# Optimization experiments

Measured on AMD Instinct MI355X. Metric: run time of the kernel, lower is better.

The kernel has to match this reference:

```python
import jax, jax.numpy as jnp
import numpy as np

N_FP = 235336   # n_fingerprint
N_WORD = 7844   # n_word
D = 10          # embed / hidden dim (hard-coded in module)
K = 23          # conv kernel 2*11+1
PAD = 11
N_ATOMS = 4096
L_WORDS = 65536


def setup_inputs() -> dict:
    key = jax.random.key(0)
    ks = jax.random.split(key, 16)
    s = 0.1  # weight init scale
    return {
        "fingerprints": jax.random.randint(ks[0], (N_ATOMS,), 0, N_FP),
        # scale adjacency so x + A@hs stays O(1) over 3 layers
        "adjacency": jax.random.uniform(ks[1], (N_ATOMS, N_ATOMS), dtype=jnp.float32) * (1.0 / N_ATOMS),
        "words": jax.random.randint(ks[2], (L_WORDS,), 0, N_WORD),
        "embed_fp": jax.random.normal(ks[3], (N_FP, D), dtype=jnp.float32) * s,
        "embed_word": jax.random.normal(ks[4], (N_WORD, D), dtype=jnp.float32) * s,
        "W_gnn_w": jax.random.normal(ks[5], (3, D, D), dtype=jnp.float32) * s,
        "W_gnn_b": jax.random.normal(ks[6], (3, D), dtype=jnp.float32) * s,
        "W_cnn_w": jax.random.normal(ks[7], (3, 1, 1, K, K), dtype=jnp.float32) * (s / K),
        "W_cnn_b": jax.random.normal(ks[8], (3,), dtype=jnp.float32) * s,
        "W_att_w": jax.random.normal(ks[9], (D, D), dtype=jnp.float32) * s,
        "W_att_b": jax.random.normal(ks[10], (D,), dtype=jnp.float32) * s,
        "W_out_w": jax.random.normal(ks[11], (3, 2 * D, 2 * D), dtype=jnp.float32) * s,
        "W_out_b": jax.random.normal(ks[12], (3, 2 * D), dtype=jnp.float32) * s,
        "W_int_w": jax.random.normal(ks[13], (2, 2 * D), dtype=jnp.float32) * s,
        "W_int_b": jax.random.normal(ks[14], (2,), dtype=jnp.float32) * s,
    }


def reference(fingerprints, adjacency, words, embed_fp, embed_word,
              W_gnn_w, W_gnn_b, W_cnn_w, W_cnn_b, W_att_w, W_att_b,
              W_out_w, W_out_b, W_int_w, W_int_b):
    # ---- Compound vector with GNN ----
    xs = embed_fp[fingerprints]                       # [N, D]
    for i in range(3):                                # fixed 3 layers
        hs = jax.nn.relu(xs @ W_gnn_w[i].T + W_gnn_b[i])
        xs = xs + adjacency @ hs                      # dense message passing
    compound = jnp.mean(xs, axis=0, keepdims=True)    # [1, D]

    # ---- Protein vector with attention-CNN ----
    ws = embed_word[words]                            # [L, D]
    t = ws[None, None]                                # [1,1,L,D] NCHW
    for i in range(3):
        t = jax.nn.relu(
            jax.lax.conv_general_dilated(t, W_cnn_w[i], (1, 1),
                                          [(PAD, PAD), (PAD, PAD)])
            + W_cnn_b[i])
    xs_p = t[0, 0]                                    # [L, D]

    h = jax.nn.relu(compound @ W_att_w.T + W_att_b)   # [1, D]
    hs_p = jax.nn.relu(xs_p @ W_att_w.T + W_att_b)    # [L, D]
    weights = jnp.tanh(h @ hs_p.T)                    # [1, L]
    ys = weights.T * hs_p                             # [L, D]
    protein = jnp.mean(ys, axis=0, keepdims=True)     # [1, D]

    # ---- Fusion MLP ----
    cat = jnp.concatenate([compound, protein], axis=1)  # [1, 2D]
    for j in range(3):
        cat = jax.nn.relu(cat @ W_out_w[j].T + W_out_b[j])
    return cat @ W_int_w.T + W_int_b                  # [1, 2]
```

## Files before the change

### kernel.cpp

```cpp
#include <hip/hip_runtime.h>
#include <math.h>

#define N_ATOMS 4096
#define L_WORDS 65536
#define DD 10
#define HALO 11

#define CONV_BLOCKS 256
#define CONV_BLOCK 256
#define GNN_BLOCKS 512
#define RPW 8
#define RPB 32
#define QCOLS 1024

__global__ __launch_bounds__(128) void gnn_embed(
    const int* __restrict__ fp, const float* __restrict__ embed_fp,
    const float* __restrict__ Wg, const float* __restrict__ bg,
    float* __restrict__ xs, float* __restrict__ hs)
{
    const int n = blockIdx.x * 128 + threadIdx.x;
    float x[DD];
    const float* e = embed_fp + (size_t)fp[n] * DD;
    #pragma unroll
    for (int d = 0; d < DD; ++d) x[d] = e[d];
    #pragma unroll
    for (int d = 0; d < DD; ++d) xs[d * N_ATOMS + n] = x[d];
    #pragma unroll
    for (int d = 0; d < DD; ++d) {
        float v = bg[d];
        #pragma unroll
        for (int k = 0; k < DD; ++k) v += Wg[d * DD + k] * x[k];
        hs[d * N_ATOMS + n] = fmaxf(v, 0.f);
    }
}

__global__ __launch_bounds__(128) void gnn_prep(
    const float* __restrict__ xs_in, const float* __restrict__ part,
    const float* __restrict__ Wg, const float* __restrict__ bg,
    float* __restrict__ xs_out, float* __restrict__ hs)
{
    const int n = blockIdx.x * 128 + threadIdx.x;
    float x[DD];
    #pragma unroll
    for (int d = 0; d < DD; ++d) {
        float v = xs_in[d * N_ATOMS + n];
        #pragma unroll
        for (int q = 0; q < 4; ++q)
            v += part[((size_t)q * DD + d) * N_ATOMS + n];
        x[d] = v;
        xs_out[d * N_ATOMS + n] = v;
    }
    #pragma unroll
    for (int d = 0; d < DD; ++d) {
        float v = bg[d];
        #pragma unroll
        for (int k = 0; k < DD; ++k) v += Wg[d * DD + k] * x[k];
        hs[d * N_ATOMS + n] = fmaxf(v, 0.f);
    }
}

__global__ __launch_bounds__(256, 3) void fused_layer(
    const float* __restrict__ A,
    const float* __restrict__ hs,
    float* __restrict__ part,
    const float* __restrict__ tin, const int* __restrict__ words,
    const float* __restrict__ embed_word, const float* __restrict__ w,
    const float* __restrict__ bptr, float* __restrict__ tout)
{
    __shared__ float sh[DD * QCOLS];
    const int tid = threadIdx.x;

    if (blockIdx.x < CONV_BLOCKS) {
        float* s = sh;
        const int l0 = blockIdx.x * CONV_BLOCK;
        for (int idx = tid; idx < (CONV_BLOCK + 2 * HALO) * DD; idx += CONV_BLOCK) {
            int rr = idx / DD, d = idx - rr * DD;
            int gr = l0 - HALO + rr;
            float v = 0.f;
            if (gr >= 0 && gr < L_WORDS) {
                if (tin) v = tin[(size_t)gr * DD + d];
                else     v = embed_word[(size_t)words[gr] * DD + d];
            }
            s[rr * 11 + d] = v;
        }
        __syncthreads();

        const float bias = *bptr;
        float acc[DD];
        #pragma unroll
        for (int d = 0; d < DD; ++d) acc[d] = bias;
        for (int i = 0; i < 23; ++i) {
            float row[DD];
            const float* sr = &s[(tid + i) * 11];
            #pragma unroll
            for (int c = 0; c < DD; ++c) row[c] = sr[c];
            #pragma unroll
            for (int d = 0; d < DD; ++d) {
                #pragma unroll
                for (int c = 0; c < DD; ++c)
                    acc[d] += row[c] * w[i * 23 + (c - d + 11)];
            }
        }
        const int l = l0 + tid;
        #pragma unroll
        for (int d = 0; d < DD; ++d)
            tout[(size_t)l * DD + d] = fmaxf(acc[d], 0.f);
    } else {
        const int b = blockIdx.x - CONV_BLOCKS;
        const int wave = tid >> 6, lane = tid & 63;
        const int q = b & 3, rg = b >> 2;

        const float4* h4 = (const float4*)hs;
        float4* shw = (float4*)sh;
        #pragma unroll
        for (int d = 0; d < DD; ++d)
            shw[d * 256 + tid] = h4[d * (N_ATOMS / 4) + q * 256 + tid];
        __syncthreads();

        const int r0 = rg * RPB + wave * RPW;
        const float4* A4 = (const float4*)(A + (size_t)r0 * N_ATOMS) + q * (QCOLS / 4);
        const float4* sh4 = (const float4*)sh;

        float acc[RPW][DD];
        #pragma unroll
        for (int r = 0; r < RPW; ++r)
            #pragma unroll
            for (int d = 0; d < DD; ++d) acc[r][d] = 0.f;

        #pragma unroll 1
        for (int it = 0; it < 4; ++it) {
            const int cb = it * 64 + lane;
            float4 a[RPW];
            #pragma unroll
            for (int r = 0; r < RPW; ++r) a[r] = A4[r * (N_ATOMS / 4) + cb];
            #pragma unroll
            for (int d = 0; d < DD; ++d) {
                float4 h = sh4[d * 256 + cb];
                #pragma unroll
                for (int r = 0; r < RPW; ++r) {
                    acc[r][d] += a[r].x * h.x;
                    acc[r][d] += a[r].y * h.y;
                    acc[r][d] += a[r].z * h.z;
                    acc[r][d] += a[r].w * h.w;
                }
            }
        }

        #pragma unroll
        for (int m = 1; m <= 4; m <<= 1) {
            #pragma unroll
            for (int r = 0; r < RPW; ++r)
                #pragma unroll
                for (int d = 0; d < DD; ++d)
                    acc[r][d] += __shfl_xor(acc[r][d], m, 64);
        }
        __syncthreads();

        if ((lane & 7) == 0) {
            const int g = lane >> 3;
            float* dst = &sh[(wave * 8 + g) * 80];
            #pragma unroll
            for (int r = 0; r < RPW; ++r)
                #pragma unroll
                for (int d = 0; d < DD; ++d) dst[r * DD + d] = acc[r][d];
        }
        __syncthreads();

        float* pdst = part + (size_t)q * DD * N_ATOMS + (size_t)rg * RPB;
        for (int o = tid; o < RPB * DD; o += 256) {
            const int d = o >> 5, rr = o & 31;
            const int w8 = rr >> 3, r = rr & 7;
            float v = 0.f;
            #pragma unroll
            for (int g = 0; g < 8; ++g) v += sh[(w8 * 8 + g) * 80 + r * DD + d];
            pdst[d * N_ATOMS + rr] = v;
        }
    }
}

__global__ __launch_bounds__(256) void comp_reduce(
    const float* __restrict__ xs, const float* __restrict__ p2,
    float* __restrict__ comp_part)
{
    const int tid = threadIdx.x, wave = tid >> 6, lane = tid & 63;
    const int n = blockIdx.x * 256 + tid;
    float x[DD];
    #pragma unroll
    for (int d = 0; d < DD; ++d) {
        float v = xs[d * N_ATOMS + n];
        #pragma unroll
        for (int qq = 0; qq < 4; ++qq)
            v += p2[((size_t)qq * DD + d) * N_ATOMS + n];
        x[d] = v;
    }
    #pragma unroll
    for (int m = 32; m >= 1; m >>= 1) {
        #pragma unroll
        for (int d = 0; d < DD; ++d) x[d] += __shfl_xor(x[d], m, 64);
    }
    __shared__ float s[4][DD];
    if (lane == 0) {
        #pragma unroll
        for (int d = 0; d < DD; ++d) s[wave][d] = x[d];
    }
    __syncthreads();
    if (tid < DD)
        comp_part[blockIdx.x * DD + tid] =
            s[0][tid] + s[1][tid] + s[2][tid] + s[3][tid];
}

__global__ __launch_bounds__(1024) void attention_pool(
    const float* __restrict__ xs_p, const float* __restrict__ comp_part,
    const float* __restrict__ Wa, const float* __restrict__ ba,
    float* __restrict__ att_part)
{
    __shared__ float shc[DD];
    __shared__ float s[16][DD];
    const int tid = threadIdx.x, wave = tid >> 6, lane = tid & 63;
    const int l = blockIdx.x * 1024 + tid;

    if (tid < DD) {
        float c = 0.f;
        #pragma unroll
        for (int p = 0; p < 16; ++p) c += comp_part[p * DD + tid];
        shc[tid] = c * (1.f / N_ATOMS);
    }
    __syncthreads();

    float h[DD];
    #pragma unroll
    for (int d = 0; d < DD; ++d) {
        float v = ba[d];
        #pragma unroll
        for (int k = 0; k < DD; ++k) v += Wa[d * DD + k] * shc[k];
        h[d] = fmaxf(v, 0.f);
    }

    float row[DD];
    #pragma unroll
    for (int d = 0; d < DD; ++d) row[d] = xs_p[(size_t)l * DD + d];

    float hp[DD], dotv = 0.f;
    #pragma unroll
    for (int d = 0; d < DD; ++d) {
        float v = ba[d];
        #pragma unroll
        for (int k = 0; k < DD; ++k) v += Wa[d * DD + k] * row[k];
        hp[d] = fmaxf(v, 0.f);
        dotv += h[d] * hp[d];
    }
    const float wgt = tanhf(dotv);

    float y[DD];
    #pragma unroll
    for (int d = 0; d < DD; ++d) y[d] = wgt * hp[d];
    #pragma unroll
    for (int m = 32; m >= 1; m >>= 1) {
        #pragma unroll
        for (int d = 0; d < DD; ++d) y[d] += __shfl_xor(y[d], m, 64);
    }
    if (lane == 0) {
        #pragma unroll
        for (int d = 0; d < DD; ++d) s[wave][d] = y[d];
    }
    __syncthreads();
    if (tid < DD) {
        float v = 0.f;
        #pragma unroll
        for (int wv = 0; wv < 16; ++wv) v += s[wv][tid];
        att_part[blockIdx.x * DD + tid] = v;
    }
}

__global__ __launch_bounds__(64) void final_mlp(
    const float* __restrict__ comp_part, const float* __restrict__ att_part,
    const float* __restrict__ Wo, const float* __restrict__ bo,
    const float* __restrict__ Wi, const float* __restrict__ bi,
    float* __restrict__ out)
{
    const int t = threadIdx.x;
    float a[DD];
    #pragma unroll
    for (int d = 0; d < DD; ++d) a[d] = att_part[t * DD + d];
    #pragma unroll
    for (int m = 32; m >= 1; m >>= 1) {
        #pragma unroll
        for (int d = 0; d < DD; ++d) a[d] += __shfl_xor(a[d], m, 64);
    }
    __shared__ float cat[20];
    if (t < DD) {
        float c = 0.f;
        #pragma unroll
        for (int p = 0; p < 16; ++p) c += comp_part[p * DD + t];
        cat[t] = c * (1.f / N_ATOMS);
    }
    if (t == 0) {
        #pragma unroll
        for (int d = 0; d < DD; ++d) cat[DD + d] = a[d] * (1.f / L_WORDS);
    }
    __syncthreads();
    for (int j = 0; j < 3; ++j) {
        float v = 0.f;
        if (t < 20) {
            v = bo[j * 20 + t];
            for (int k = 0; k < 20; ++k) v += Wo[j * 400 + t * 20 + k] * cat[k];
        }
        __syncthreads();
        if (t < 20) cat[t] = fmaxf(v, 0.f);
        __syncthreads();
    }
    if (t < 2) {
        float v = bi[t];
        for (int k = 0; k < 20; ++k) v += Wi[t * 20 + k] * cat[k];
        out[t] = v;
    }
}

extern "C" void kernel_launch(void* const* d_in, const int* in_sizes, int n_in,
                              void* d_out, int out_size, void* d_ws, size_t ws_size,
                              hipStream_t stream)
{
    const int*   fp     = (const int*)d_in[0];
    const float* A      = (const float*)d_in[1];
    const int*   words  = (const int*)d_in[2];
    const float* emb_fp = (const float*)d_in[3];
    const float* emb_w  = (const float*)d_in[4];
    const float* Wg     = (const float*)d_in[5];
    const float* bg     = (const float*)d_in[6];
    const float* Wc     = (const float*)d_in[7];
    const float* bc     = (const float*)d_in[8];
    const float* Wa     = (const float*)d_in[9];
    const float* ba     = (const float*)d_in[10];
    const float* Wo     = (const float*)d_in[11];
    const float* bo     = (const float*)d_in[12];
    const float* Wi     = (const float*)d_in[13];
    const float* bi     = (const float*)d_in[14];
    float* out = (float*)d_out;
    float* ws  = (float*)d_ws;

    float* xs0   = ws;
    float* xs1   = ws + 40960;
    float* xs2   = ws + 81920;
    float* hs    = ws + 122880;
    float* ta    = ws + 163840;
    float* tb    = ws + 819200;
    float* part0 = ws + 1474560;
    float* part1 = ws + 1638400;
    float* part2 = ws + 1802240;
    float* comp_part = ws + 1966080;
    float* att_part  = ws + 1966240;

    const int fused_grid = CONV_BLOCKS + GNN_BLOCKS;

    gnn_embed<<<N_ATOMS / 128, 128, 0, stream>>>(fp, emb_fp, Wg, bg, xs0, hs);

    fused_layer<<<fused_grid, 256, 0, stream>>>(
        A, hs, part0, nullptr, words, emb_w, Wc, bc, ta);

    gnn_prep<<<N_ATOMS / 128, 128, 0, stream>>>(
        xs0, part0, Wg + 100, bg + 10, xs1, hs);

    fused_layer<<<fused_grid, 256, 0, stream>>>(
        A, hs, part1, ta, words, emb_w, Wc + 529, bc + 1, tb);

    gnn_prep<<<N_ATOMS / 128, 128, 0, stream>>>(
        xs1, part1, Wg + 200, bg + 20, xs2, hs);

    fused_layer<<<fused_grid, 256, 0, stream>>>(
        A, hs, part2, tb, words, emb_w, Wc + 1058, bc + 2, ta);

    comp_reduce<<<16, 256, 0, stream>>>(xs2, part2, comp_part);

    attention_pool<<<L_WORDS / 1024, 1024, 0, stream>>>(
        ta, comp_part, Wa, ba, att_part);

    final_mlp<<<1, 64, 0, stream>>>(comp_part, att_part, Wo, bo, Wi, bi, out);
}
```

Baseline: 206.5 us.

## Fuse GNN prep into layer kernel and merge attention with final MLP

Each GNN block now recomputes the x update and hs = relu(W x + b) for its column quarter directly into shared memory, which removes the separate gnn_embed and gnn_prep launches and the hs round trip through global memory. The last conv layer also applies the attention projection and writes hp directly. comp_reduce, attention_pool and final_mlp become one kernel: every block redundantly recomputes the compound mean, and the last-arriving block, chosen by an atomic ticket, runs the MLP. The cost is redundant prep work (each of 128 row groups recomputes hs for its quarter), a memset launch for the ticket, and relaxed atomics without an explicit release fence.

```diff
diff --git a/kernel.cpp b/kernel.cpp
--- a/kernel.cpp
+++ b/kernel.cpp
@@ -8,222 +8,239 @@
 
 #define CONV_BLOCKS 256
 #define CONV_BLOCK 256
-#define GNN_BLOCKS 512
 #define RPW 8
 #define RPB 32
 #define QCOLS 1024
-
-__global__ __launch_bounds__(128) void gnn_embed(
-    const int* __restrict__ fp, const float* __restrict__ embed_fp,
-    const float* __restrict__ Wg, const float* __restrict__ bg,
-    float* __restrict__ xs, float* __restrict__ hs)
-{
-    const int n = blockIdx.x * 128 + threadIdx.x;
-    float x[DD];
-    const float* e = embed_fp + (size_t)fp[n] * DD;
-    #pragma unroll
-    for (int d = 0; d < DD; ++d) x[d] = e[d];
-    #pragma unroll
-    for (int d = 0; d < DD; ++d) xs[d * N_ATOMS + n] = x[d];
-    #pragma unroll
-    for (int d = 0; d < DD; ++d) {
-        float v = bg[d];
-        #pragma unroll
-        for (int k = 0; k < DD; ++k) v += Wg[d * DD + k] * x[k];
-        hs[d * N_ATOMS + n] = fmaxf(v, 0.f);
-    }
-}
-
-__global__ __launch_bounds__(128) void gnn_prep(
-    const float* __restrict__ xs_in, const float* __restrict__ part,
-    const float* __restrict__ Wg, const float* __restrict__ bg,
-    float* __restrict__ xs_out, float* __restrict__ hs)
-{
-    const int n = blockIdx.x * 128 + threadIdx.x;
-    float x[DD];
-    #pragma unroll
-    for (int d = 0; d < DD; ++d) {
-        float v = xs_in[d * N_ATOMS + n];
-        #pragma unroll
-        for (int q = 0; q < 4; ++q)
-            v += part[((size_t)q * DD + d) * N_ATOMS + n];
-        x[d] = v;
-        xs_out[d * N_ATOMS + n] = v;
-    }
-    #pragma unroll
-    for (int d = 0; d < DD; ++d) {
-        float v = bg[d];
-        #pragma unroll
-        for (int k = 0; k < DD; ++k) v += Wg[d * DD + k] * x[k];
-        hs[d * N_ATOMS + n] = fmaxf(v, 0.f);
-    }
-}
-
-__global__ __launch_bounds__(256, 3) void fused_layer(
-    const float* __restrict__ A,
-    const float* __restrict__ hs,
-    float* __restrict__ part,
+#define TOTAL_BLOCKS 768
+#define ATT_BLOCKS 64
+
+__device__ __forceinline__ void conv_stage(
+    float* sh, const int tid, const int bx,
     const float* __restrict__ tin, const int* __restrict__ words,
     const float* __restrict__ embed_word, const float* __restrict__ w,
-    const float* __restrict__ bptr, float* __restrict__ tout)
+    const float* __restrict__ bptr, float* __restrict__ tout,
+    const float* __restrict__ Wa, const float* __restrict__ ba,
+    float* __restrict__ hpb)
+{
+    const int l0 = bx * CONV_BLOCK;
+    for (int idx = tid; idx < (CONV_BLOCK + 2 * HALO) * DD; idx += CONV_BLOCK) {
+        int rr = idx / DD, d = idx - rr * DD;
+        int gr = l0 - HALO + rr;
+        float v = 0.f;
+        if (gr >= 0 && gr < L_WORDS) {
+            if (tin) v = tin[(size_t)gr * DD + d];
+            else     v = embed_word[(size_t)words[gr] * DD + d];
+        }
+        sh[rr * 11 + d] = v;
+    }
+    __syncthreads();
+
+    const float bias = *bptr;
+    float acc[DD];
+    #pragma unroll
+    for (int d = 0; d < DD; ++d) acc[d] = bias;
+    for (int i = 0; i < 23; ++i) {
+        float row[DD];
+        const float* sr = &sh[(tid + i) * 11];
+        #pragma unroll
+        for (int c = 0; c < DD; ++c) row[c] = sr[c];
+        #pragma unroll
+        for (int d = 0; d < DD; ++d) {
+            #pragma unroll
+            for (int c = 0; c < DD; ++c)
+                acc[d] += row[c] * w[i * 23 + (c - d + 11)];
+        }
+    }
+    const int l = l0 + tid;
+    if (tout) {
+        #pragma unroll
+        for (int d = 0; d < DD; ++d)
+            tout[(size_t)l * DD + d] = fmaxf(acc[d], 0.f);
+    }
+    if (hpb) {
+        float xsp[DD];
+        #pragma unroll
+        for (int d = 0; d < DD; ++d) xsp[d] = fmaxf(acc[d], 0.f);
+        #pragma unroll
+        for (int d = 0; d < DD; ++d) {
+            float v = ba[d];
+            #pragma unroll
+            for (int k = 0; k < DD; ++k) v += Wa[d * DD + k] * xsp[k];
+            hpb[(size_t)l * DD + d] = fmaxf(v, 0.f);
+        }
+    }
+}
+
+__device__ __forceinline__ void gnn_stage(
+    float* sh, const int tid, const int b,
+    const int* __restrict__ fp, const float* __restrict__ emb_fp,
+    const float* __restrict__ xs_in, const float* __restrict__ part_in,
+    const float* __restrict__ Wg, const float* __restrict__ bg,
+    float* __restrict__ xs_out,
+    const float* __restrict__ A, float* __restrict__ part_out)
+{
+    const int wave = tid >> 6, lane = tid & 63;
+    const int q = b & 3, rg = b >> 2;
+    const int qbase = q * QCOLS;
+
+    for (int j = 0; j < 4; ++j) {
+        const int lc = j * 256 + tid;
+        const int n = qbase + lc;
+        float x[DD];
+        if (xs_in) {
+            #pragma unroll
+            for (int d = 0; d < DD; ++d) {
+                float v = xs_in[d * N_ATOMS + n];
+                #pragma unroll
+                for (int qq = 0; qq < 4; ++qq)
+                    v += part_in[((size_t)qq * DD + d) * N_ATOMS + n];
+                x[d] = v;
+            }
+        } else {
+            const float* e = emb_fp + (size_t)fp[n] * DD;
+            #pragma unroll
+            for (int d = 0; d < DD; ++d) x[d] = e[d];
+        }
+        if (rg == 0) {
+            #pragma unroll
+            for (int d = 0; d < DD; ++d) xs_out[d * N_ATOMS + n] = x[d];
+        }
+        #pragma unroll
+        for (int d = 0; d < DD; ++d) {
+            float v = bg[d];
+            #pragma unroll
+            for (int k = 0; k < DD; ++k) v += Wg[d * DD + k] * x[k];
+            sh[d * QCOLS + lc] = fmaxf(v, 0.f);
+        }
+    }
+    __syncthreads();
+
+    const int r0 = rg * RPB + wave * RPW;
+    const float4* A4 = (const float4*)(A + (size_t)r0 * N_ATOMS) + q * (QCOLS / 4);
+    const float4* sh4 = (const float4*)sh;
+
+    float acc[RPW][DD];
+    #pragma unroll
+    for (int r = 0; r < RPW; ++r)
+        #pragma unroll
+        for (int d = 0; d < DD; ++d) acc[r][d] = 0.f;
+
+    #pragma unroll 1
+    for (int it = 0; it < 4; ++it) {
+        const int cb = it * 64 + lane;
+        float4 a[RPW];
+        #pragma unroll
+        for (int r = 0; r < RPW; ++r) a[r] = A4[r * (N_ATOMS / 4) + cb];
+        #pragma unroll
+        for (int d = 0; d < DD; ++d) {
+            float4 h = sh4[d * 256 + cb];
+            #pragma unroll
+            for (int r = 0; r < RPW; ++r) {
+                acc[r][d] += a[r].x * h.x;
+                acc[r][d] += a[r].y * h.y;
+                acc[r][d] += a[r].z * h.z;
+                acc[r][d] += a[r].w * h.w;
+            }
+        }
+    }
+
+    #pragma unroll
+    for (int m = 1; m <= 4; m <<= 1) {
+        #pragma unroll
+        for (int r = 0; r < RPW; ++r)
+            #pragma unroll
+            for (int d = 0; d < DD; ++d)
+                acc[r][d] += __shfl_xor(acc[r][d], m, 64);
+    }
+    __syncthreads();
+
+    if ((lane & 7) == 0) {
+        const int g = lane >> 3;
+        float* dst = &sh[(wave * 8 + g) * 80];
+        #pragma unroll
+        for (int r = 0; r < RPW; ++r)
+            #pragma unroll
+            for (int d = 0; d < DD; ++d) dst[r * DD + d] = acc[r][d];
+    }
+    __syncthreads();
+
+    float* pdst = part_out + (size_t)q * DD * N_ATOMS + (size_t)rg * RPB;
+    for (int o = tid; o < RPB * DD; o += 256) {
+        const int d = o >> 5, rr = o & 31;
+        const int w8 = rr >> 3, r = rr & 7;
+        float v = 0.f;
+        #pragma unroll
+        for (int g = 0; g < 8; ++g) v += sh[(w8 * 8 + g) * 80 + r * DD + d];
+        pdst[d * N_ATOMS + rr] = v;
+    }
+}
+
+__global__ __launch_bounds__(256, 3) void fused_layer(
+    const float* __restrict__ A, const int* __restrict__ fp,
+    const float* __restrict__ emb_fp,
+    const float* __restrict__ xs_in, const float* __restrict__ part_in,
+    const float* __restrict__ Wg, const float* __restrict__ bg,
+    float* __restrict__ xs_out, float* __restrict__ part_out,
+    const float* __restrict__ tin, const int* __restrict__ words,
+    const float* __restrict__ emb_w, const float* __restrict__ wc,
+    const float* __restrict__ bc, float* __restrict__ tout,
+    const float* __restrict__ Wa, const float* __restrict__ ba,
+    float* __restrict__ hpb)
 {
     __shared__ float sh[DD * QCOLS];
     const int tid = threadIdx.x;
-
-    if (blockIdx.x < CONV_BLOCKS) {
-        float* s = sh;
-        const int l0 = blockIdx.x * CONV_BLOCK;
-        for (int idx = tid; idx < (CONV_BLOCK + 2 * HALO) * DD; idx += CONV_BLOCK) {
-            int rr = idx / DD, d = idx - rr * DD;
-            int gr = l0 - HALO + rr;
-            float v = 0.f;
-            if (gr >= 0 && gr < L_WORDS) {
-                if (tin) v = tin[(size_t)gr * DD + d];
-                else     v = embed_word[(size_t)words[gr] * DD + d];
-            }
-            s[rr * 11 + d] = v;
-        }
-        __syncthreads();
-
-        const float bias = *bptr;
-        float acc[DD];
-        #pragma unroll
-        for (int d = 0; d < DD; ++d) acc[d] = bias;
-        for (int i = 0; i < 23; ++i) {
-            float row[DD];
-            const float* sr = &s[(tid + i) * 11];
-            #pragma unroll
-            for (int c = 0; c < DD; ++c) row[c] = sr[c];
-            #pragma unroll
-            for (int d = 0; d < DD; ++d) {
-                #pragma unroll
-                for (int c = 0; c < DD; ++c)
-                    acc[d] += row[c] * w[i * 23 + (c - d + 11)];
-            }
-        }
-        const int l = l0 + tid;
-        #pragma unroll
-        for (int d = 0; d < DD; ++d)
-            tout[(size_t)l * DD + d] = fmaxf(acc[d], 0.f);
-    } else {
-        const int b = blockIdx.x - CONV_BLOCKS;
-        const int wave = tid >> 6, lane = tid & 63;
-        const int q = b & 3, rg = b >> 2;
-
-        const float4* h4 = (const float4*)hs;
-        float4* shw = (float4*)sh;
-        #pragma unroll
-        for (int d = 0; d < DD; ++d)
-            shw[d * 256 + tid] = h4[d * (N_ATOMS / 4) + q * 256 + tid];
-        __syncthreads();
-
-        const int r0 = rg * RPB + wave * RPW;
-        const float4* A4 = (const float4*)(A + (size_t)r0 * N_ATOMS) + q * (QCOLS / 4);
-        const float4* sh4 = (const float4*)sh;
-
-        float acc[RPW][DD];
-        #pragma unroll
-        for (int r = 0; r < RPW; ++r)
-            #pragma unroll
-            for (int d = 0; d < DD; ++d) acc[r][d] = 0.f;
-
-        #pragma unroll 1
-        for (int it = 0; it < 4; ++it) {
-            const int cb = it * 64 + lane;
-            float4 a[RPW];
-            #pragma unroll
-            for (int r = 0; r < RPW; ++r) a[r] = A4[r * (N_ATOMS / 4) + cb];
-            #pragma unroll
-            for (int d = 0; d < DD; ++d) {
-                float4 h = sh4[d * 256 + cb];
-                #pragma unroll
-                for (int r = 0; r < RPW; ++r) {
-                    acc[r][d] += a[r].x * h.x;
-                    acc[r][d] += a[r].y * h.y;
-                    acc[r][d] += a[r].z * h.z;
-                    acc[r][d] += a[r].w * h.w;
-                }
-            }
-        }
-
-        #pragma unroll
-        for (int m = 1; m <= 4; m <<= 1) {
-            #pragma unroll
-            for (int r = 0; r < RPW; ++r)
-                #pragma unroll
-                for (int d = 0; d < DD; ++d)
-                    acc[r][d] += __shfl_xor(acc[r][d], m, 64);
-        }
-        __syncthreads();
-
-        if ((lane & 7) == 0) {
-            const int g = lane >> 3;
-            float* dst = &sh[(wave * 8 + g) * 80];
-            #pragma unroll
-            for (int r = 0; r < RPW; ++r)
-                #pragma unroll
-                for (int d = 0; d < DD; ++d) dst[r * DD + d] = acc[r][d];
-        }
-        __syncthreads();
-
-        float* pdst = part + (size_t)q * DD * N_ATOMS + (size_t)rg * RPB;
-        for (int o = tid; o < RPB * DD; o += 256) {
-            const int d = o >> 5, rr = o & 31;
-            const int w8 = rr >> 3, r = rr & 7;
-            float v = 0.f;
-            #pragma unroll
-            for (int g = 0; g < 8; ++g) v += sh[(w8 * 8 + g) * 80 + r * DD + d];
-            pdst[d * N_ATOMS + rr] = v;
-        }
-    }
-}
-
-__global__ __launch_bounds__(256) void comp_reduce(
-    const float* __restrict__ xs, const float* __restrict__ p2,
-    float* __restrict__ comp_part)
-{
+    if (blockIdx.x < CONV_BLOCKS)
+        conv_stage(sh, tid, blockIdx.x, tin, words, emb_w, wc, bc, tout,
+                   Wa, ba, hpb);
+    else
+        gnn_stage(sh, tid, blockIdx.x - CONV_BLOCKS, fp, emb_fp,
+                  xs_in, part_in, Wg, bg, xs_out, A, part_out);
+}
+
+__global__ __launch_bounds__(1024) void attn_final(
+    const float* __restrict__ xs2, const float* __restrict__ part2,
+    const float* __restrict__ hpb,
+    const float* __restrict__ Wa, const float* __restrict__ ba,
+    const float* __restrict__ Wo, const float* __restrict__ bo,
+    const float* __restrict__ Wi, const float* __restrict__ bi,
+    float* att_part, unsigned int* ticket, float* __restrict__ out)
+{
+    __shared__ float red[16][DD];
+    __shared__ float shc[DD];
+    __shared__ float cat[20];
+    __shared__ int islast;
     const int tid = threadIdx.x, wave = tid >> 6, lane = tid & 63;
-    const int n = blockIdx.x * 256 + tid;
-    float x[DD];
-    #pragma unroll
-    for (int d = 0; d < DD; ++d) {
-        float v = xs[d * N_ATOMS + n];
-        #pragma unroll
-        for (int qq = 0; qq < 4; ++qq)
-            v += p2[((size_t)qq * DD + d) * N_ATOMS + n];
-        x[d] = v;
+
+    float c[DD];
+    #pragma unroll
+    for (int d = 0; d < DD; ++d) c[d] = 0.f;
+    #pragma unroll
+    for (int s = 0; s < 4; ++s) {
+        const int n = s * 1024 + tid;
+        #pragma unroll
+        for (int d = 0; d < DD; ++d) {
+            float v = xs2[d * N_ATOMS + n];
+            #pragma unroll
+            for (int qq = 0; qq < 4; ++qq)
+                v += part2[((size_t)qq * DD + d) * N_ATOMS + n];
+            c[d] += v;
+        }
     }
     #pragma unroll
     for (int m = 32; m >= 1; m >>= 1) {
         #pragma unroll
-        for (int d = 0; d < DD; ++d) x[d] += __shfl_xor(x[d], m, 64);
-    }
-    __shared__ float s[4][DD];
+        for (int d = 0; d < DD; ++d) c[d] += __shfl_xor(c[d], m, 64);
+    }
     if (lane == 0) {
         #pragma unroll
-        for (int d = 0; d < DD; ++d) s[wave][d] = x[d];
-    }
-    __syncthreads();
-    if (tid < DD)
-        comp_part[blockIdx.x * DD + tid] =
-            s[0][tid] + s[1][tid] + s[2][tid] + s[3][tid];
-}
-
-__global__ __launch_bounds__(1024) void attention_pool(
-    const float* __restrict__ xs_p, const float* __restrict__ comp_part,
-    const float* __restrict__ Wa, const float* __restrict__ ba,
-    float* __restrict__ att_part)
-{
-    __shared__ float shc[DD];
-    __shared__ float s[16][DD];
-    const int tid = threadIdx.x, wave = tid >> 6, lane = tid & 63;
-    const int l = blockIdx.x * 1024 + tid;
-
+        for (int d = 0; d < DD; ++d) red[wave][d] = c[d];
+    }
+    __syncthreads();
     if (tid < DD) {
-        float c = 0.f;
-        #pragma unroll
-        for (int p = 0; p < 16; ++p) c += comp_part[p * DD + tid];
-        shc[tid] = c * (1.f / N_ATOMS);
+        float v = 0.f;
+        #pragma unroll
+        for (int w = 0; w < 16; ++w) v += red[w][tid];
+        shc[tid] = v * (1.f / N_ATOMS);
     }
     __syncthreads();
 
@@ -235,22 +252,14 @@
         for (int k = 0; k < DD; ++k) v += Wa[d * DD + k] * shc[k];
         h[d] = fmaxf(v, 0.f);
     }
-
-    float row[DD];
-    #pragma unroll
-    for (int d = 0; d < DD; ++d) row[d] = xs_p[(size_t)l * DD + d];
-
+    const int w_ = blockIdx.x * 1024 + tid;
     float hp[DD], dotv = 0.f;
     #pragma unroll
     for (int d = 0; d < DD; ++d) {
-        float v = ba[d];
-        #pragma unroll
-        for (int k = 0; k < DD; ++k) v += Wa[d * DD + k] * row[k];
-        hp[d] = fmaxf(v, 0.f);
+        hp[d] = hpb[(size_t)w_ * DD + d];
         dotv += h[d] * hp[d];
     }
     const float wgt = tanhf(dotv);
-
     float y[DD];
     #pragma unroll
     for (int d = 0; d < DD; ++d) y[d] = wgt * hp[d];
@@ -259,60 +268,66 @@
         #pragma unroll
         for (int d = 0; d < DD; ++d) y[d] += __shfl_xor(y[d], m, 64);
     }
+    __syncthreads();
     if (lane == 0) {
         #pragma unroll
-        for (int d = 0; d < DD; ++d) s[wave][d] = y[d];
+        for (int d = 0; d < DD; ++d) red[wave][d] = y[d];
     }
     __syncthreads();
     if (tid < DD) {
         float v = 0.f;
         #pragma unroll
-        for (int wv = 0; wv < 16; ++wv) v += s[wv][tid];
-        att_part[blockIdx.x * DD + tid] = v;
-    }
-}
-
-__global__ __launch_bounds__(64) void final_mlp(
-    const float* __restrict__ comp_part, const float* __restrict__ att_part,
-    const float* __restrict__ Wo, const float* __restrict__ bo,
-    const float* __restrict__ Wi, const float* __restrict__ bi,
-    float* __restrict__ out)
-{
-    const int t = threadIdx.x;
+        for (int w = 0; w < 16; ++w) v += red[w][tid];
+        __hip_atomic_store(att_part + blockIdx.x * DD + tid, v,
+                           __ATOMIC_RELAXED, __HIP_MEMORY_SCOPE_AGENT);
+    }
+    __syncthreads();
+
+    if (tid == 0) {
+        unsigned prev = __hip_atomic_fetch_add(ticket, 1u, __ATOMIC_RELAXED,
+                                               __HIP_MEMORY_SCOPE_AGENT);
+        islast = (prev == ATT_BLOCKS - 1);
+    }
+    __syncthreads();
+    if (!islast) return;
+    asm volatile("" ::: "memory");
+
     float a[DD];
     #pragma unroll
-    for (int d = 0; d < DD; ++d) a[d] = att_part[t * DD + d];
-    #pragma unroll
-    for (int m = 32; m >= 1; m >>= 1) {
-        #pragma unroll
-        for (int d = 0; d < DD; ++d) a[d] += __shfl_xor(a[d], m, 64);
-    }
-    __shared__ float cat[20];
-    if (t < DD) {
-        float c = 0.f;
-        #pragma unroll
-        for (int p = 0; p < 16; ++p) c += comp_part[p * DD + t];
-        cat[t] = c * (1.f / N_ATOMS);
-    }
-    if (t == 0) {
+    for (int d = 0; d < DD; ++d) a[d] = 0.f;
+    if (tid < ATT_BLOCKS) {
+        #pragma unroll
+        for (int d = 0; d < DD; ++d)
+            a[d] = __hip_atomic_load(att_part + tid * DD + d,
+                                     __ATOMIC_RELAXED, __HIP_MEMORY_SCOPE_AGENT);
+    }
+    if (wave == 0) {
+        #pragma unroll
+        for (int m = 32; m >= 1; m >>= 1) {
+            #pragma unroll
+            for (int d = 0; d < DD; ++d) a[d] += __shfl_xor(a[d], m, 64);
+        }
+    }
+    if (tid == 0) {
         #pragma unroll
         for (int d = 0; d < DD; ++d) cat[DD + d] = a[d] * (1.f / L_WORDS);
     }
+    if (tid < DD) cat[tid] = shc[tid];
     __syncthreads();
     for (int j = 0; j < 3; ++j) {
         float v = 0.f;
-        if (t < 20) {
-            v = bo[j * 20 + t];
-            for (int k = 0; k < 20; ++k) v += Wo[j * 400 + t * 20 + k] * cat[k];
+        if (tid < 20) {
+            v = bo[j * 20 + tid];
+            for (int k = 0; k < 20; ++k) v += Wo[j * 400 + tid * 20 + k] * cat[k];
         }
         __syncthreads();
-        if (t < 20) cat[t] = fmaxf(v, 0.f);
+        if (tid < 20) cat[tid] = fmaxf(v, 0.f);
         __syncthreads();
     }
-    if (t < 2) {
-        float v = bi[t];
-        for (int k = 0; k < 20; ++k) v += Wi[t * 20 + k] * cat[k];
-        out[t] = v;
+    if (tid < 2) {
+        float v = bi[tid];
+        for (int k = 0; k < 20; ++k) v += Wi[tid * 20 + k] * cat[k];
+        out[tid] = v;
     }
 }
 
@@ -341,38 +356,29 @@
     float* xs0   = ws;
     float* xs1   = ws + 40960;
     float* xs2   = ws + 81920;
-    float* hs    = ws + 122880;
-    float* ta    = ws + 163840;
-    float* tb    = ws + 819200;
-    float* part0 = ws + 1474560;
-    float* part1 = ws + 1638400;
-    float* part2 = ws + 1802240;
-    float* comp_part = ws + 1966080;
-    float* att_part  = ws + 1966240;
-
-    const int fused_grid = CONV_BLOCKS + GNN_BLOCKS;
-
-    gnn_embed<<<N_ATOMS / 128, 128, 0, stream>>>(fp, emb_fp, Wg, bg, xs0, hs);
-
-    fused_layer<<<fused_grid, 256, 0, stream>>>(
-        A, hs, part0, nullptr, words, emb_w, Wc, bc, ta);
-
-    gnn_prep<<<N_ATOMS / 128, 128, 0, stream>>>(
-        xs0, part0, Wg + 100, bg + 10, xs1, hs);
-
-    fused_layer<<<fused_grid, 256, 0, stream>>>(
-        A, hs, part1, ta, words, emb_w, Wc + 529, bc + 1, tb);
-
-    gnn_prep<<<N_ATOMS / 128, 128, 0, stream>>>(
-        xs1, part1, Wg + 200, bg + 20, xs2, hs);
-
-    fused_layer<<<fused_grid, 256, 0, stream>>>(
-        A, hs, part2, tb, words, emb_w, Wc + 1058, bc + 2, ta);
-
-    comp_reduce<<<16, 256, 0, stream>>>(xs2, part2, comp_part);
-
-    attention_pool<<<L_WORDS / 1024, 1024, 0, stream>>>(
-        ta, comp_part, Wa, ba, att_part);
-
-    final_mlp<<<1, 64, 0, stream>>>(comp_part, att_part, Wo, bo, Wi, bi, out);
-}
+    float* part0 = ws + 122880;
+    float* part1 = ws + 286720;
+    float* part2 = ws + 450560;
+    float* ta    = ws + 614400;
+    float* tb    = ws + 1269760;
+    float* hpb   = ta;
+    float* att_part = ws + 1925120;
+    unsigned int* ticket = (unsigned int*)(ws + 1925760);
+
+    hipMemsetAsync(ticket, 0, sizeof(unsigned int), stream);
+
+    fused_layer<<<TOTAL_BLOCKS, 256, 0, stream>>>(
+        A, fp, emb_fp, nullptr, nullptr, Wg, bg, xs0, part0,
+        nullptr, words, emb_w, Wc, bc, ta, nullptr, nullptr, nullptr);
+
+    fused_layer<<<TOTAL_BLOCKS, 256, 0, stream>>>(
+        A, fp, emb_fp, xs0, part0, Wg + 100, bg + 10, xs1, part1,
+        ta, words, emb_w, Wc + 529, bc + 1, tb, nullptr, nullptr, nullptr);
+
+    fused_layer<<<TOTAL_BLOCKS, 256, 0, stream>>>(
+        A, fp, emb_fp, xs1, part1, Wg + 200, bg + 20, xs2, part2,
+        tb, words, emb_w, Wc + 1058, bc + 2, nullptr, Wa, ba, hpb);
+
+    attn_final<<<ATT_BLOCKS, 1024, 0, stream>>>(
+        xs2, part2, hpb, Wa, ba, Wo, bo, Wi, bi, att_part, ticket, out);
+}
```

Result: slower. 212.5 us (+2.9%).
